# Performance work log

Hardware: AMD Instinct MI355X
Metric: run time of the kernel (lower is better)

## Reference

```python
import jax, jax.numpy as jnp
import numpy as np

N = 100_000      # num nodes
E = 1_600_000    # num edges
F_IN = 128       # input feature dim
H = 128          # hidden dim
C = 16           # num classes
R = 5            # num relations


def setup_inputs() -> dict:
    key = jax.random.key(0)
    ks = jax.random.split(key, 12)
    x = jax.random.normal(ks[0], (N, F_IN), jnp.float32)
    edge_index = jax.random.randint(ks[1], (2, E), 0, N, dtype=jnp.int64)
    edge_weight = jax.random.uniform(ks[2], (E,), jnp.float32)
    edge_type = jax.random.randint(ks[3], (E,), 0, R, dtype=jnp.int64)
    # RGCNConv params (no basis decomposition): per-relation weight, root, bias
    s1 = 1.0 / np.sqrt(F_IN).astype(np.float32)
    s2 = 1.0 / np.sqrt(H).astype(np.float32)
    W1 = jax.random.normal(ks[4], (R, F_IN, H), jnp.float32) * s1
    root1 = jax.random.normal(ks[5], (F_IN, H), jnp.float32) * s1
    b1 = jnp.zeros((H,), jnp.float32)
    W2 = jax.random.normal(ks[6], (R, H, C), jnp.float32) * s2
    root2 = jax.random.normal(ks[7], (H, C), jnp.float32) * s2
    b2 = jnp.zeros((C,), jnp.float32)
    return {"x": x, "edge_index": edge_index, "edge_weight": edge_weight,
            "edge_type": edge_type, "W1": W1, "root1": root1, "b1": b1,
            "W2": W2, "root2": root2, "b2": b2}


def _rgcn_conv(x, src, dst, ew, et, W, root, b):
    """WeightedRGCNConv: per-relation weighted mean aggregation + relation matmul.

    Equivalent to the torch loop over relations: mask edges of type r,
    propagate with aggr='mean' (PyG RGCNConv default) on messages
    edge_weight * x[src], then h_r @ W[r], summed over r; plus root & bias.
    Vectorized by scattering into (dst, relation) buckets.
    """
    n, r = x.shape[0], W.shape[0]
    m = x[src] * ew[:, None]                       # [E, d_in] messages
    seg = dst * r + et                             # bucket = (dst node, relation)
    sums = jax.ops.segment_sum(m, seg, num_segments=n * r).reshape(n, r, -1)
    cnt = jax.ops.segment_sum(jnp.ones_like(ew), seg, num_segments=n * r)
    cnt = cnt.reshape(n, r, 1)
    agg = sums / jnp.maximum(cnt, 1.0)             # mean; 0 for empty buckets
    out = jnp.einsum('nri,rio->no', agg, W)        # sum_r H_r @ W_r
    return out + x @ root + b


def reference(x, edge_index, edge_weight, edge_type, W1, root1, b1, W2, root2, b2):
    src, dst = edge_index[0], edge_index[1]
    h = _rgcn_conv(x, src, dst, edge_weight, edge_type, W1, root1, b1)
    h = jax.nn.relu(h)  # dropout is identity in eval mode
    out = _rgcn_conv(h, src, dst, edge_weight, edge_type, W2, root2, b2)
    return jax.nn.log_softmax(out, axis=1)
```

## Files before the change

### kernel.cpp

```cpp
#include <hip/hip_runtime.h>

#define N_NODES 100000
#define N_EDGES 1600000
#define N_REL   5
#define NCOARSE  196
#define CAP      16384

using bf16x8 = __attribute__((ext_vector_type(8))) short;
using f32x4  = __attribute__((ext_vector_type(4))) float;
using f32x2  = __attribute__((ext_vector_type(2))) float;

__device__ __forceinline__ unsigned short f2bf(float f) {
    unsigned int u = __float_as_uint(f);
    u += 0x7fffu + ((u >> 16) & 1u);
    return (unsigned short)(u >> 16);
}
__device__ __forceinline__ float bfu(unsigned short u) { return __uint_as_float((unsigned int)u << 16); }

__global__ __launch_bounds__(1024) void partition_append(
    const int* __restrict__ src, const int* __restrict__ dstv,
    const float* __restrict__ ew, const int* __restrict__ et,
    int* __restrict__ ccur, int2* __restrict__ pe) {
    __shared__ int lh[256];
    __shared__ int lb[256];
    int tid = threadIdx.x;
    if (tid < 256) lh[tid] = 0;
    __syncthreads();
    int base = blockIdx.x * 4096;
    int key[4], rank[4], meta[4];
    float w[4];
    #pragma unroll
    for (int i = 0; i < 4; ++i) {
        int e = base + i * 1024 + tid;
        key[i] = -1;
        if (e < N_EDGES) {
            int d = dstv[e];
            key[i] = d >> 9;
            meta[i] = src[e] | (et[e] << 17) | ((d & 511) << 20);
            w[i] = ew[e];
            rank[i] = atomicAdd(&lh[key[i]], 1);
        }
    }
    __syncthreads();
    if (tid < 256) {
        int c = lh[tid];
        lb[tid] = c ? atomicAdd(&ccur[tid], c) : 0;
    }
    __syncthreads();
    #pragma unroll
    for (int i = 0; i < 4; ++i)
        if (key[i] >= 0) {
            int pos = lb[key[i]] + rank[i];
            if (pos < CAP)
                pe[((size_t)key[i] << 14) + pos] = make_int2(meta[i], __float_as_int(w[i]));
        }
}

__global__ __launch_bounds__(256) void cscan(const int* __restrict__ ccur,
                                             int* __restrict__ cstart) {
    __shared__ int lds[256];
    int tid = threadIdx.x;
    int v = ccur[tid];
    lds[tid] = v;
    __syncthreads();
    for (int d = 1; d < 256; d <<= 1) {
        int t = (tid >= d) ? lds[tid - d] : 0;
        __syncthreads();
        lds[tid] += t;
        __syncthreads();
    }
    cstart[tid] = lds[tid] - v;
}

__global__ __launch_bounds__(1024) void bucket_sort(
    const int* __restrict__ ccnt, const int* __restrict__ cstart,
    const int2* __restrict__ pe, int2* __restrict__ edges,
    int* __restrict__ nbase, int2* __restrict__ nbp) {
    int cb = blockIdx.x;
    int node0 = cb << 9;
    if (node0 >= N_NODES) return;
    int nNodes = N_NODES - node0; if (nNodes > 512) nNodes = 512;
    int nf = nNodes * N_REL;
    __shared__ int hist[2560];
    __shared__ int cur[2560];
    __shared__ int wtot[16];
    __shared__ int woff[16];
    int tid = threadIdx.x;
    int wid = tid >> 6, lane = tid & 63;
    int cnt = ccnt[cb]; if (cnt > CAP) cnt = CAP;
    int gbase = cstart[cb];
    const int2* my = pe + ((size_t)cb << 14);

    for (int i = tid; i < nf; i += 1024) hist[i] = 0;
    __syncthreads();
    for (int i = tid; i < cnt; i += 1024) {
        int m = my[i].x;
        atomicAdd(&hist[((m >> 20) & 511) * N_REL + ((m >> 17) & 7)], 1);
    }
    __syncthreads();

    int t0 = tid * 3;
    int a0 = (t0 + 0 < nf) ? hist[t0 + 0] : 0;
    int a1 = (t0 + 1 < nf) ? hist[t0 + 1] : 0;
    int a2 = (t0 + 2 < nf) ? hist[t0 + 2] : 0;
    int s = a0 + a1 + a2;
    int incl = s;
    #pragma unroll
    for (int d = 1; d < 64; d <<= 1) {
        int t = __shfl_up(incl, d);
        if (lane >= d) incl += t;
    }
    if (lane == 63) wtot[wid] = incl;
    __syncthreads();
    if (wid == 0 && lane < 16) {
        int v = wtot[lane];
        int inc2 = v;
        #pragma unroll
        for (int d = 1; d < 16; d <<= 1) {
            int t = __shfl_up(inc2, d);
            if (lane >= d) inc2 += t;
        }
        woff[lane] = inc2 - v;
    }
    __syncthreads();
    int excl = incl - s + woff[wid];
    if (t0 + 0 < nf) cur[t0 + 0] = excl;
    excl += a0;
    if (t0 + 1 < nf) cur[t0 + 1] = excl;
    excl += a1;
    if (t0 + 2 < nf) cur[t0 + 2] = excl;
    __syncthreads();

    for (int i = tid; i < nNodes; i += 1024) {
        int b = i * N_REL;
        int c0 = cur[b];
        int deg = cur[b + 4] + hist[b + 4] - c0;
        nbase[node0 + i] = gbase + c0;
        nbp[node0 + i] = make_int2(0, deg);
    }
    __syncthreads();

    for (int i = tid; i < cnt; i += 1024) {
        int2 r = my[i];
        int fb = ((r.x >> 20) & 511) * N_REL + ((r.x >> 17) & 7);
        int pos = gbase + atomicAdd(&cur[fb], 1);
        float wf = __int_as_float(r.y) / (float)hist[fb];
        edges[pos] = make_int2(r.x & 0xFFFFF, __float_as_int(wf));
    }
}

__global__ void cvt_feat(const float* __restrict__ x, ushort* __restrict__ xh) {
    int i = blockIdx.x * blockDim.x + threadIdx.x;
    if (i >= (N_NODES * 128) / 4) return;
    float4 v = reinterpret_cast<const float4*>(x)[i];
    ushort4 o;
    o.x = f2bf(v.x); o.y = f2bf(v.y); o.z = f2bf(v.z); o.w = f2bf(v.w);
    reinterpret_cast<ushort4*>(xh)[i] = o;
}

__global__ void cvt_w1b(const float* __restrict__ W1, ushort* __restrict__ Wt1b) {
    int i = blockIdx.x * blockDim.x + threadIdx.x;
    if (i >= 640 * 128) return;
    int o640 = i >> 7, k = i & 127;
    int r = o640 >> 7, o = o640 & 127;
    Wt1b[i] = f2bf(W1[((size_t)r * 128 + k) * 128 + o]);
}

__global__ void cvt_root(const float* __restrict__ root1, ushort* __restrict__ Wtroot) {
    int i = blockIdx.x * blockDim.x + threadIdx.x;
    if (i >= 128 * 128) return;
    int o = i >> 7, k = i & 127;
    Wtroot[i] = f2bf(root1[k * 128 + o]);
}

__global__ void cvt_w2(const float* __restrict__ W2, const float* __restrict__ root2,
                       ushort* __restrict__ Wt2s) {
    int i = blockIdx.x * blockDim.x + threadIdx.x;
    if (i >= 96 * 128) return;
    int o = i >> 7, k = i & 127;
    float v = (o < 16) ? root2[k * 16 + o]
                       : W2[((size_t)((o >> 4) - 1) * 128 + k) * 16 + (o & 15)];
    Wt2s[i] = f2bf(v);
}

__global__ __launch_bounds__(256) void gemmZ(
    const ushort* __restrict__ xh, const ushort* __restrict__ Wt1b,
    unsigned char* __restrict__ Zq) {
    __shared__ ushort As[128 * 128];
    __shared__ ushort Bs[128 * 128];
    const int tid = threadIdx.x, lane = tid & 63, wave = tid >> 6;
    const int m0 = blockIdx.x * 128;

    #pragma unroll
    for (int u = 0; u < 8; ++u) {
        int idx = tid + u * 256;
        int row = idx >> 4, slot = idx & 15;
        int gr = m0 + row; if (gr >= N_NODES) gr = N_NODES - 1;
        float4 v = *reinterpret_cast<const float4*>(xh + (size_t)gr * 128 + slot * 8);
        int byte = row * 256 + ((slot ^ (row & 15)) << 4);
        *reinterpret_cast<float4*>(reinterpret_cast<char*>(As) + byte) = v;
    }

    for (int seg = 0; seg < 5; ++seg) {
        #pragma unroll
        for (int u = 0; u < 8; ++u) {
            int idx = tid + u * 256;
            int row = idx >> 4, slot = idx & 15;
            float4 v = *reinterpret_cast<const float4*>(
                Wt1b + ((size_t)(seg * 128 + row)) * 128 + slot * 8);
            int byte = row * 256 + ((slot ^ (row & 15)) << 4);
            *reinterpret_cast<float4*>(reinterpret_cast<char*>(Bs) + byte) = v;
        }
        __syncthreads();

        f32x4 acc[2][8] = {};
        #pragma unroll
        for (int ks = 0; ks < 4; ++ks) {
            bf16x8 af[2], bfr[8];
            #pragma unroll
            for (int m = 0; m < 2; ++m) {
                int row = wave * 32 + m * 16 + (lane & 15);
                int slot = ks * 4 + (lane >> 4);
                int byte = row * 256 + ((slot ^ (row & 15)) << 4);
                af[m] = *reinterpret_cast<const bf16x8*>(
                    reinterpret_cast<const char*>(As) + byte);
            }
            #pragma unroll
            for (int nn = 0; nn < 8; ++nn) {
                int row = nn * 16 + (lane & 15);
                int slot = ks * 4 + (lane >> 4);
                int byte = row * 256 + ((slot ^ (row & 15)) << 4);
                bfr[nn] = *reinterpret_cast<const bf16x8*>(
                    reinterpret_cast<const char*>(Bs) + byte);
            }
            #pragma unroll
            for (int m = 0; m < 2; ++m)
                #pragma unroll
                for (int nn = 0; nn < 8; ++nn)
                    acc[m][nn] = __builtin_amdgcn_mfma_f32_16x16x32_bf16(
                        af[m], bfr[nn], acc[m][nn], 0, 0, 0);
        }

        #pragma unroll
        for (int m = 0; m < 2; ++m) {
            int rloc = m0 + wave * 32 + m * 16 + (lane >> 4) * 4;
            #pragma unroll
            for (int nn = 0; nn < 8; ++nn) {
                int c = seg * 128 + nn * 16 + (lane & 15);
                #pragma unroll
                for (int q = 0; q < 4; ++q) {
                    int row = rloc + q;
                    if (row < N_NODES) {
                        float v = acc[m][nn][q];
                        int p = __builtin_amdgcn_cvt_pk_fp8_f32(v, v, 0, false);
                        Zq[(size_t)row * 640 + c] = (unsigned char)(p & 0xFF);
                    }
                }
            }
        }
        __syncthreads();
    }
}

__global__ __launch_bounds__(256) void gather2(
    const ushort* __restrict__ Zq,
    const int2* __restrict__ edges,
    const int* __restrict__ nbase, const int2* __restrict__ nbp,
    ushort* __restrict__ hpre) {
    int n = __builtin_amdgcn_readfirstlane(blockIdx.x * 4 + (threadIdx.x >> 6));
    int lane = threadIdx.x & 63;
    int o0  = __builtin_amdgcn_readfirstlane(nbase[n]);
    int deg = __builtin_amdgcn_readfirstlane(nbp[n].y);
    float ax = 0.f, ay = 0.f;

    if (deg <= 64) {
        int2 er = (lane < deg) ? edges[o0 + lane] : make_int2(0, 0);
        int deg8 = (deg + 7) & ~7;
        for (int j = 0; j < deg8; j += 8) {
            unsigned short q[8];
            float w[8];
            #pragma unroll
            for (int u = 0; u < 8; ++u) {
                int m = __builtin_amdgcn_readlane(er.x, j + u);
                int s5 = (m & 0x1FFFF) * 5 + ((m >> 17) & 7);
                q[u] = Zq[((size_t)s5 << 6) + lane];
            }
            #pragma unroll
            for (int u = 0; u < 8; ++u)
                w[u] = __uint_as_float(__builtin_amdgcn_readlane(er.y, j + u));
            #pragma unroll
            for (int u = 0; u < 8; ++u) {
                f32x2 f = __builtin_amdgcn_cvt_pk_f32_fp8((int)q[u], false);
                ax = fmaf(w[u], f.x, ax); ay = fmaf(w[u], f.y, ay);
            }
        }
    } else {
        for (int base = o0; base < o0 + deg; base += 64) {
            int rem = o0 + deg - base;
            int mcap = rem > 64 ? 64 : rem;
            int2 er = (lane < mcap) ? edges[base + lane] : make_int2(0, 0);
            int m8 = (mcap + 7) & ~7;
            for (int j = 0; j < m8; j += 8) {
                unsigned short q[8];
                float w[8];
                #pragma unroll
                for (int u = 0; u < 8; ++u) {
                    int m = __builtin_amdgcn_readlane(er.x, j + u);
                    int s5 = (m & 0x1FFFF) * 5 + ((m >> 17) & 7);
                    q[u] = Zq[((size_t)s5 << 6) + lane];
                }
                #pragma unroll
                for (int u = 0; u < 8; ++u)
                    w[u] = __uint_as_float(__builtin_amdgcn_readlane(er.y, j + u));
                #pragma unroll
                for (int u = 0; u < 8; ++u) {
                    f32x2 f = __builtin_amdgcn_cvt_pk_f32_fp8((int)q[u], false);
                    ax = fmaf(w[u], f.x, ax); ay = fmaf(w[u], f.y, ay);
                }
            }
        }
    }

    reinterpret_cast<unsigned int*>(hpre)[(size_t)n * 64 + lane] =
        (unsigned int)f2bf(ax) | ((unsigned int)f2bf(ay) << 16);
}

__global__ __launch_bounds__(256) void gemmL1fr(
    const ushort* __restrict__ xh,
    const ushort* __restrict__ Wtroot,
    const float* __restrict__ bias,
    const ushort* __restrict__ hpre,
    const ushort* __restrict__ Wt2,
    ushort* __restrict__ Yh) {
    __shared__ ushort As[128 * 128];
    __shared__ ushort Bs[128 * 128];
    const int tid = threadIdx.x, lane = tid & 63, wave = tid >> 6;
    const int m0 = blockIdx.x * 128;

    #pragma unroll
    for (int u = 0; u < 8; ++u) {
        int idx = tid + u * 256;
        int row = idx >> 4, slot = idx & 15;
        int gr = m0 + row; if (gr >= N_NODES) gr = N_NODES - 1;
        float4 v = *reinterpret_cast<const float4*>(xh + (size_t)gr * 128 + slot * 8);
        int byte = row * 256 + ((slot ^ (row & 15)) << 4);
        *reinterpret_cast<float4*>(reinterpret_cast<char*>(As) + byte) = v;
    }
    #pragma unroll
    for (int u = 0; u < 8; ++u) {
        int idx = tid + u * 256;
        int row = idx >> 4, slot = idx & 15;
        float4 v = *reinterpret_cast<const float4*>(Wtroot + (size_t)row * 128 + slot * 8);
        int byte = row * 256 + ((slot ^ (row & 15)) << 4);
        *reinterpret_cast<float4*>(reinterpret_cast<char*>(Bs) + byte) = v;
    }
    __syncthreads();

    f32x4 acc[2][8] = {};
    #pragma unroll
    for (int ks = 0; ks < 4; ++ks) {
        bf16x8 af[2], bfr[8];
        #pragma unroll
        for (int m = 0; m < 2; ++m) {
            int row = wave * 32 + m * 16 + (lane & 15);
            int slot = ks * 4 + (lane >> 4);
            int byte = row * 256 + ((slot ^ (row & 15)) << 4);
            af[m] = *reinterpret_cast<const bf16x8*>(
                reinterpret_cast<const char*>(As) + byte);
        }
        #pragma unroll
        for (int nn = 0; nn < 8; ++nn) {
            int row = nn * 16 + (lane & 15);
            int slot = ks * 4 + (lane >> 4);
            int byte = row * 256 + ((slot ^ (row & 15)) << 4);
            bfr[nn] = *reinterpret_cast<const bf16x8*>(
                reinterpret_cast<const char*>(Bs) + byte);
        }
        #pragma unroll
        for (int m = 0; m < 2; ++m)
            #pragma unroll
            for (int nn = 0; nn < 8; ++nn)
                acc[m][nn] = __builtin_amdgcn_mfma_f32_16x16x32_bf16(
                    af[m], bfr[nn], acc[m][nn], 0, 0, 0);
    }
    __syncthreads();

    #pragma unroll
    for (int m = 0; m < 2; ++m) {
        int rloc = wave * 32 + m * 16 + (lane >> 4) * 4;
        #pragma unroll
        for (int nn = 0; nn < 8; ++nn) {
            int c = nn * 16 + (lane & 15);
            float bv = bias[c];
            #pragma unroll
            for (int q = 0; q < 4; ++q) {
                int row = rloc + q;
                int grow = m0 + row; if (grow >= N_NODES) grow = N_NODES - 1;
                float v = fmaxf(acc[m][nn][q] + bv +
                                bfu(hpre[(size_t)grow * 128 + c]), 0.f);
                int byte = row * 256 + ((((c >> 3) ^ (row & 15)) << 4)) + (c & 7) * 2;
                *reinterpret_cast<ushort*>(reinterpret_cast<char*>(As) + byte) = f2bf(v);
            }
        }
    }
    __syncthreads();

    f32x4 acc2[2][6] = {};
    #pragma unroll
    for (int ks = 0; ks < 4; ++ks) {
        bf16x8 af[2], bfr[6];
        #pragma unroll
        for (int m = 0; m < 2; ++m) {
            int row = wave * 32 + m * 16 + (lane & 15);
            int slot = ks * 4 + (lane >> 4);
            int byte = row * 256 + ((slot ^ (row & 15)) << 4);
            af[m] = *reinterpret_cast<const bf16x8*>(
                reinterpret_cast<const char*>(As) + byte);
        }
        #pragma unroll
        for (int nn = 0; nn < 6; ++nn) {
            int row = nn * 16 + (lane & 15);
            int slot = ks * 4 + (lane >> 4);
            bfr[nn] = *reinterpret_cast<const bf16x8*>(
                Wt2 + (size_t)row * 128 + slot * 8);
        }
        #pragma unroll
        for (int m = 0; m < 2; ++m)
            #pragma unroll
            for (int nn = 0; nn < 6; ++nn)
                acc2[m][nn] = __builtin_amdgcn_mfma_f32_16x16x32_bf16(
                    af[m], bfr[nn], acc2[m][nn], 0, 0, 0);
    }

    #pragma unroll
    for (int m = 0; m < 2; ++m) {
        int rloc = wave * 32 + m * 16 + (lane >> 4) * 4;
        #pragma unroll
        for (int nn = 0; nn < 6; ++nn) {
            int c = nn * 16 + (lane & 15);
            #pragma unroll
            for (int q = 0; q < 4; ++q) {
                int grow = m0 + rloc + q;
                if (grow < N_NODES)
                    Yh[(size_t)grow * 96 + c] = f2bf(acc2[m][nn][q]);
            }
        }
    }
}

__global__ __launch_bounds__(256) void agg2_softmax(
    const ushort* __restrict__ Yh, const int2* __restrict__ edges,
    const int* __restrict__ nbase, const int2* __restrict__ nbp,
    const float* __restrict__ b2, float* __restrict__ out) {
    int wave = threadIdx.x >> 6, lane = threadIdx.x & 63;
    int q = lane >> 4, c = lane & 15;
    int n = (blockIdx.x * 4 + wave) * 4 + q;
    int nn = (n < N_NODES) ? n : N_NODES - 1;
    int o0 = nbase[nn];
    int deg = nbp[nn].y;

    float val = bfu(Yh[(size_t)nn * 96 + c]) + b2[c];

    for (int b = 0; b < deg; b += 16) {
        int2 er = (b + c < deg) ? edges[o0 + b + c] : make_int2(0, 0);
        #pragma unroll
        for (int j = 0; j < 16; ++j) {
            int m = __shfl(er.x, q * 16 + j);
            float w = __uint_as_float(__shfl(er.y, q * 16 + j));
            int s = m & 0x1FFFF;
            int rel = (m >> 17) & 7;
            val = fmaf(w, bfu(Yh[(size_t)s * 96 + 16 + rel * 16 + c]), val);
        }
    }

    float mx = val;
    #pragma unroll
    for (int i = 1; i < 16; i <<= 1) mx = fmaxf(mx, __shfl_xor(mx, i));
    float ex = expf(val - mx);
    float ssum = ex;
    #pragma unroll
    for (int i = 1; i < 16; i <<= 1) ssum += __shfl_xor(ssum, i);
    float r = val - mx - logf(ssum);
    if (n < N_NODES) out[(size_t)n * 16 + c] = r;
}

extern "C" void kernel_launch(void* const* d_in, const int* in_sizes, int n_in,
                              void* d_out, int out_size, void* d_ws, size_t ws_size,
                              hipStream_t stream) {
    const float* x     = (const float*)d_in[0];
    const int*   ei    = (const int*)d_in[1];
    const int*   src   = ei;
    const int*   dst   = ei + N_EDGES;
    const float* ew    = (const float*)d_in[2];
    const int*   et    = (const int*)d_in[3];
    const float* W1    = (const float*)d_in[4];
    const float* root1 = (const float*)d_in[5];
    const float* b1    = (const float*)d_in[6];
    const float* W2    = (const float*)d_in[7];
    const float* root2 = (const float*)d_in[8];
    const float* b2    = (const float*)d_in[9];
    float* out = (float*)d_out;

    char* ws = (char*)d_ws;
    int*    ccur    = (int*)ws;
    int*    cstart  = (int*)(ws + 1024);
    int*    nbase   = (int*)(ws + 4096);
    int2*   nbp     = (int2*)(ws + 404096);
    int2*   edges   = (int2*)(ws + 1204096);
    ushort* xh      = (ushort*)(ws + 14004096);
    ushort* Wt1b    = (ushort*)(ws + 39604096);
    ushort* Wtroot  = (ushort*)(ws + 39767936);
    ushort* Wt2s    = (ushort*)(ws + 39800704);
    ushort* hpre    = (ushort*)(ws + 39825280);
    unsigned char* Zq = (unsigned char*)(ws + 65425280);
    ushort* Yh      = (ushort*)(ws + 129425280);
    int2*   pe      = (int2*)(ws + 148625280);

    cvt_feat<<<((N_NODES * 128 / 4) + 255) / 256, 256, 0, stream>>>(x, xh);
    cvt_w1b<<<(640 * 128 + 255) / 256, 256, 0, stream>>>(W1, Wt1b);
    cvt_root<<<(128 * 128 + 255) / 256, 256, 0, stream>>>(root1, Wtroot);
    cvt_w2<<<(96 * 128 + 255) / 256, 256, 0, stream>>>(W2, root2, Wt2s);

    hipMemsetAsync(ccur, 0, 1024, stream);
    partition_append<<<(N_EDGES + 4095) / 4096, 1024, 0, stream>>>(src, dst, ew, et, ccur, pe);
    cscan<<<1, 256, 0, stream>>>(ccur, cstart);
    bucket_sort<<<NCOARSE, 1024, 0, stream>>>(ccur, cstart, pe, edges, nbase, nbp);

    gemmZ<<<(N_NODES + 127) / 128, 256, 0, stream>>>(xh, Wt1b, Zq);

    gather2<<<N_NODES / 4, 256, 0, stream>>>(
        (const ushort*)Zq, edges, nbase, nbp, hpre);

    gemmL1fr<<<(N_NODES + 127) / 128, 256, 0, stream>>>(
        xh, Wtroot, b1, hpre, Wt2s, Yh);

    agg2_softmax<<<(N_NODES + 15) / 16, 256, 0, stream>>>(
        Yh, edges, nbase, nbp, b2, out);
}
```

Baseline: 205.8 us.

## Fold root GEMM into first-layer GEMM and fuse bias/ReLU into gather

The root weight is appended as a sixth 128-column segment of the layer-1 weight matrix, so gemmZ computes x@root1 alongside the relation projections and writes it as bf16. The gather kernel then adds this root term, the bias and ReLU, and writes the hidden activation directly, leaving the second-layer GEMM as a simple h@W2 kernel. gemmZ and gemmYh also stop staging the B operand in shared memory and read weights straight from global memory, which removes a sync per segment. The cost is an extra bf16 Zroot buffer written and read back, and uncoalesced global B-fragment loads that depend on cache hits.

```diff
diff --git a/kernel.cpp b/kernel.cpp
--- a/kernel.cpp
+++ b/kernel.cpp
@@ -16,6 +16,8 @@
     return (unsigned short)(u >> 16);
 }
 __device__ __forceinline__ float bfu(unsigned short u) { return __uint_as_float((unsigned int)u << 16); }
+__device__ __forceinline__ float bflo(unsigned int p) { return __uint_as_float(p << 16); }
+__device__ __forceinline__ float bfhi(unsigned int p) { return __uint_as_float(p & 0xffff0000u); }
 
 __global__ __launch_bounds__(1024) void partition_append(
     const int* __restrict__ src, const int* __restrict__ dstv,
@@ -158,19 +160,19 @@
     reinterpret_cast<ushort4*>(xh)[i] = o;
 }
 
-__global__ void cvt_w1b(const float* __restrict__ W1, ushort* __restrict__ Wt1b) {
+__global__ void cvt_w1b(const float* __restrict__ W1, const float* __restrict__ root1,
+                        ushort* __restrict__ Wt1b) {
     int i = blockIdx.x * blockDim.x + threadIdx.x;
-    if (i >= 640 * 128) return;
+    if (i >= 768 * 128) return;
     int o640 = i >> 7, k = i & 127;
-    int r = o640 >> 7, o = o640 & 127;
-    Wt1b[i] = f2bf(W1[((size_t)r * 128 + k) * 128 + o]);
-}
-
-__global__ void cvt_root(const float* __restrict__ root1, ushort* __restrict__ Wtroot) {
-    int i = blockIdx.x * blockDim.x + threadIdx.x;
-    if (i >= 128 * 128) return;
-    int o = i >> 7, k = i & 127;
-    Wtroot[i] = f2bf(root1[k * 128 + o]);
+    float v;
+    if (o640 < 640) {
+        int r = o640 >> 7, o = o640 & 127;
+        v = W1[((size_t)r * 128 + k) * 128 + o];
+    } else {
+        v = root1[k * 128 + (o640 - 640)];
+    }
+    Wt1b[i] = f2bf(v);
 }
 
 __global__ void cvt_w2(const float* __restrict__ W2, const float* __restrict__ root2,
@@ -185,9 +187,8 @@
 
 __global__ __launch_bounds__(256) void gemmZ(
     const ushort* __restrict__ xh, const ushort* __restrict__ Wt1b,
-    unsigned char* __restrict__ Zq) {
+    unsigned char* __restrict__ Zq, ushort* __restrict__ Zroot) {
     __shared__ ushort As[128 * 128];
-    __shared__ ushort Bs[128 * 128];
     const int tid = threadIdx.x, lane = tid & 63, wave = tid >> 6;
     const int m0 = blockIdx.x * 128;
 
@@ -200,19 +201,9 @@
         int byte = row * 256 + ((slot ^ (row & 15)) << 4);
         *reinterpret_cast<float4*>(reinterpret_cast<char*>(As) + byte) = v;
     }
-
-    for (int seg = 0; seg < 5; ++seg) {
-        #pragma unroll
-        for (int u = 0; u < 8; ++u) {
-            int idx = tid + u * 256;
-            int row = idx >> 4, slot = idx & 15;
-            float4 v = *reinterpret_cast<const float4*>(
-                Wt1b + ((size_t)(seg * 128 + row)) * 128 + slot * 8);
-            int byte = row * 256 + ((slot ^ (row & 15)) << 4);
-            *reinterpret_cast<float4*>(reinterpret_cast<char*>(Bs) + byte) = v;
-        }
-        __syncthreads();
-
+    __syncthreads();
+
+    for (int seg = 0; seg < 6; ++seg) {
         f32x4 acc[2][8] = {};
         #pragma unroll
         for (int ks = 0; ks < 4; ++ks) {
@@ -227,11 +218,9 @@
             }
             #pragma unroll
             for (int nn = 0; nn < 8; ++nn) {
-                int row = nn * 16 + (lane & 15);
-                int slot = ks * 4 + (lane >> 4);
-                int byte = row * 256 + ((slot ^ (row & 15)) << 4);
+                int brow = seg * 128 + nn * 16 + (lane & 15);
                 bfr[nn] = *reinterpret_cast<const bf16x8*>(
-                    reinterpret_cast<const char*>(Bs) + byte);
+                    Wt1b + (size_t)brow * 128 + (ks * 4 + (lane >> 4)) * 8);
             }
             #pragma unroll
             for (int m = 0; m < 2; ++m)
@@ -246,19 +235,23 @@
             int rloc = m0 + wave * 32 + m * 16 + (lane >> 4) * 4;
             #pragma unroll
             for (int nn = 0; nn < 8; ++nn) {
-                int c = seg * 128 + nn * 16 + (lane & 15);
+                int c = nn * 16 + (lane & 15);
                 #pragma unroll
                 for (int q = 0; q < 4; ++q) {
                     int row = rloc + q;
                     if (row < N_NODES) {
                         float v = acc[m][nn][q];
-                        int p = __builtin_amdgcn_cvt_pk_fp8_f32(v, v, 0, false);
-                        Zq[(size_t)row * 640 + c] = (unsigned char)(p & 0xFF);
+                        if (seg < 5) {
+                            int p = __builtin_amdgcn_cvt_pk_fp8_f32(v, v, 0, false);
+                            Zq[(size_t)row * 640 + seg * 128 + c] =
+                                (unsigned char)(p & 0xFF);
+                        } else {
+                            Zroot[(size_t)row * 128 + c] = f2bf(v);
+                        }
                     }
                 }
             }
         }
-        __syncthreads();
     }
 }
 
@@ -266,7 +259,9 @@
     const ushort* __restrict__ Zq,
     const int2* __restrict__ edges,
     const int* __restrict__ nbase, const int2* __restrict__ nbp,
-    ushort* __restrict__ hpre) {
+    const ushort* __restrict__ Zroot,
+    const float* __restrict__ b1,
+    ushort* __restrict__ h) {
     int n = __builtin_amdgcn_readfirstlane(blockIdx.x * 4 + (threadIdx.x >> 6));
     int lane = threadIdx.x & 63;
     int o0  = __builtin_amdgcn_readfirstlane(nbase[n]);
@@ -321,19 +316,17 @@
         }
     }
 
-    reinterpret_cast<unsigned int*>(hpre)[(size_t)n * 64 + lane] =
-        (unsigned int)f2bf(ax) | ((unsigned int)f2bf(ay) << 16);
-}
-
-__global__ __launch_bounds__(256) void gemmL1fr(
-    const ushort* __restrict__ xh,
-    const ushort* __restrict__ Wtroot,
-    const float* __restrict__ bias,
-    const ushort* __restrict__ hpre,
-    const ushort* __restrict__ Wt2,
+    unsigned int zr = reinterpret_cast<const unsigned int*>(Zroot)[(size_t)n * 64 + lane];
+    float h0 = fmaxf(bflo(zr) + ax + b1[2 * lane], 0.f);
+    float h1 = fmaxf(bfhi(zr) + ay + b1[2 * lane + 1], 0.f);
+    reinterpret_cast<unsigned int*>(h)[(size_t)n * 64 + lane] =
+        (unsigned int)f2bf(h0) | ((unsigned int)f2bf(h1) << 16);
+}
+
+__global__ __launch_bounds__(256) void gemmYh(
+    const ushort* __restrict__ h, const ushort* __restrict__ Wt2,
     ushort* __restrict__ Yh) {
     __shared__ ushort As[128 * 128];
-    __shared__ ushort Bs[128 * 128];
     const int tid = threadIdx.x, lane = tid & 63, wave = tid >> 6;
     const int m0 = blockIdx.x * 128;
 
@@ -342,24 +335,16 @@
         int idx = tid + u * 256;
         int row = idx >> 4, slot = idx & 15;
         int gr = m0 + row; if (gr >= N_NODES) gr = N_NODES - 1;
-        float4 v = *reinterpret_cast<const float4*>(xh + (size_t)gr * 128 + slot * 8);
+        float4 v = *reinterpret_cast<const float4*>(h + (size_t)gr * 128 + slot * 8);
         int byte = row * 256 + ((slot ^ (row & 15)) << 4);
         *reinterpret_cast<float4*>(reinterpret_cast<char*>(As) + byte) = v;
     }
-    #pragma unroll
-    for (int u = 0; u < 8; ++u) {
-        int idx = tid + u * 256;
-        int row = idx >> 4, slot = idx & 15;
-        float4 v = *reinterpret_cast<const float4*>(Wtroot + (size_t)row * 128 + slot * 8);
-        int byte = row * 256 + ((slot ^ (row & 15)) << 4);
-        *reinterpret_cast<float4*>(reinterpret_cast<char*>(Bs) + byte) = v;
-    }
-    __syncthreads();
-
-    f32x4 acc[2][8] = {};
+    __syncthreads();
+
+    f32x4 acc2[2][6] = {};
     #pragma unroll
     for (int ks = 0; ks < 4; ++ks) {
-        bf16x8 af[2], bfr[8];
+        bf16x8 af[2], bfr[6];
         #pragma unroll
         for (int m = 0; m < 2; ++m) {
             int row = wave * 32 + m * 16 + (lane & 15);
@@ -369,60 +354,10 @@
                 reinterpret_cast<const char*>(As) + byte);
         }
         #pragma unroll
-        for (int nn = 0; nn < 8; ++nn) {
-            int row = nn * 16 + (lane & 15);
-            int slot = ks * 4 + (lane >> 4);
-            int byte = row * 256 + ((slot ^ (row & 15)) << 4);
-            bfr[nn] = *reinterpret_cast<const bf16x8*>(
-                reinterpret_cast<const char*>(Bs) + byte);
-        }
-        #pragma unroll
-        for (int m = 0; m < 2; ++m)
-            #pragma unroll
-            for (int nn = 0; nn < 8; ++nn)
-                acc[m][nn] = __builtin_amdgcn_mfma_f32_16x16x32_bf16(
-                    af[m], bfr[nn], acc[m][nn], 0, 0, 0);
-    }
-    __syncthreads();
-
-    #pragma unroll
-    for (int m = 0; m < 2; ++m) {
-        int rloc = wave * 32 + m * 16 + (lane >> 4) * 4;
-        #pragma unroll
-        for (int nn = 0; nn < 8; ++nn) {
-            int c = nn * 16 + (lane & 15);
-            float bv = bias[c];
-            #pragma unroll
-            for (int q = 0; q < 4; ++q) {
-                int row = rloc + q;
-                int grow = m0 + row; if (grow >= N_NODES) grow = N_NODES - 1;
-                float v = fmaxf(acc[m][nn][q] + bv +
-                                bfu(hpre[(size_t)grow * 128 + c]), 0.f);
-                int byte = row * 256 + ((((c >> 3) ^ (row & 15)) << 4)) + (c & 7) * 2;
-                *reinterpret_cast<ushort*>(reinterpret_cast<char*>(As) + byte) = f2bf(v);
-            }
-        }
-    }
-    __syncthreads();
-
-    f32x4 acc2[2][6] = {};
-    #pragma unroll
-    for (int ks = 0; ks < 4; ++ks) {
-        bf16x8 af[2], bfr[6];
-        #pragma unroll
-        for (int m = 0; m < 2; ++m) {
-            int row = wave * 32 + m * 16 + (lane & 15);
-            int slot = ks * 4 + (lane >> 4);
-            int byte = row * 256 + ((slot ^ (row & 15)) << 4);
-            af[m] = *reinterpret_cast<const bf16x8*>(
-                reinterpret_cast<const char*>(As) + byte);
-        }
-        #pragma unroll
         for (int nn = 0; nn < 6; ++nn) {
             int row = nn * 16 + (lane & 15);
-            int slot = ks * 4 + (lane >> 4);
             bfr[nn] = *reinterpret_cast<const bf16x8*>(
-                Wt2 + (size_t)row * 128 + slot * 8);
+                Wt2 + (size_t)row * 128 + (ks * 4 + (lane >> 4)) * 8);
         }
         #pragma unroll
         for (int m = 0; m < 2; ++m)
@@ -434,15 +369,14 @@
 
     #pragma unroll
     for (int m = 0; m < 2; ++m) {
-        int rloc = wave * 32 + m * 16 + (lane >> 4) * 4;
+        int rloc = m0 + wave * 32 + m * 16 + (lane >> 4) * 4;
         #pragma unroll
         for (int nn = 0; nn < 6; ++nn) {
             int c = nn * 16 + (lane & 15);
             #pragma unroll
             for (int q = 0; q < 4; ++q) {
-                int grow = m0 + rloc + q;
-                if (grow < N_NODES)
-                    Yh[(size_t)grow * 96 + c] = f2bf(acc2[m][nn][q]);
+                int row = rloc + q;
+                if (row < N_NODES) Yh[(size_t)row * 96 + c] = f2bf(acc2[m][nn][q]);
             }
         }
     }
@@ -509,16 +443,15 @@
     int2*   edges   = (int2*)(ws + 1204096);
     ushort* xh      = (ushort*)(ws + 14004096);
     ushort* Wt1b    = (ushort*)(ws + 39604096);
-    ushort* Wtroot  = (ushort*)(ws + 39767936);
     ushort* Wt2s    = (ushort*)(ws + 39800704);
-    ushort* hpre    = (ushort*)(ws + 39825280);
-    unsigned char* Zq = (unsigned char*)(ws + 65425280);
-    ushort* Yh      = (ushort*)(ws + 129425280);
-    int2*   pe      = (int2*)(ws + 148625280);
+    ushort* Zroot   = (ushort*)(ws + 39825280);
+    ushort* h       = (ushort*)(ws + 65425280);
+    unsigned char* Zq = (unsigned char*)(ws + 91025280);
+    ushort* Yh      = (ushort*)(ws + 155025280);
+    int2*   pe      = (int2*)(ws + 174225280);
 
     cvt_feat<<<((N_NODES * 128 / 4) + 255) / 256, 256, 0, stream>>>(x, xh);
-    cvt_w1b<<<(640 * 128 + 255) / 256, 256, 0, stream>>>(W1, Wt1b);
-    cvt_root<<<(128 * 128 + 255) / 256, 256, 0, stream>>>(root1, Wtroot);
+    cvt_w1b<<<(768 * 128 + 255) / 256, 256, 0, stream>>>(W1, root1, Wt1b);
     cvt_w2<<<(96 * 128 + 255) / 256, 256, 0, stream>>>(W2, root2, Wt2s);
 
     hipMemsetAsync(ccur, 0, 1024, stream);
@@ -526,13 +459,12 @@
     cscan<<<1, 256, 0, stream>>>(ccur, cstart);
     bucket_sort<<<NCOARSE, 1024, 0, stream>>>(ccur, cstart, pe, edges, nbase, nbp);
 
-    gemmZ<<<(N_NODES + 127) / 128, 256, 0, stream>>>(xh, Wt1b, Zq);
+    gemmZ<<<(N_NODES + 127) / 128, 256, 0, stream>>>(xh, Wt1b, Zq, Zroot);
 
     gather2<<<N_NODES / 4, 256, 0, stream>>>(
-        (const ushort*)Zq, edges, nbase, nbp, hpre);
-
-    gemmL1fr<<<(N_NODES + 127) / 128, 256, 0, stream>>>(
-        xh, Wtroot, b1, hpre, Wt2s, Yh);
+        (const ushort*)Zq, edges, nbase, nbp, Zroot, b1, h);
+
+    gemmYh<<<(N_NODES + 127) / 128, 256, 0, stream>>>(h, Wt2s, Yh);
 
     agg2_softmax<<<(N_NODES + 15) / 16, 256, 0, stream>>>(
         Yh, edges, nbase, nbp, b2, out);
```

Result: slower. 274.2 us (+33.2%).
